# Optimization experiments

Hardware: AMD Instinct MI355X
Metric: run time of the kernel (lower is better)

## Reference

```python
import jax, jax.numpy as jnp
import numpy as np

N_SRC0, N_DST0, N_E0 = 286000, 11000, 275000
N_DST1, N_E1 = 1000, 10000
IN_FEATS, N_HIDDEN, N_CLASSES = 602, 256, 41


def setup_inputs() -> dict:
    key = jax.random.key(0)
    ks = jax.random.split(key, 12)
    inp = {
        "x": jax.random.normal(ks[0], (N_SRC0, IN_FEATS), dtype=jnp.float32),
        "Wself0": jax.random.normal(ks[1], (IN_FEATS, N_HIDDEN), dtype=jnp.float32) * 0.05,
        "Wneigh0": jax.random.normal(ks[2], (IN_FEATS, N_HIDDEN), dtype=jnp.float32) * 0.05,
        "b0": jnp.zeros((N_HIDDEN,), dtype=jnp.float32),
        "Wself1": jax.random.normal(ks[3], (N_HIDDEN, N_CLASSES), dtype=jnp.float32) * 0.05,
        "Wneigh1": jax.random.normal(ks[4], (N_HIDDEN, N_CLASSES), dtype=jnp.float32) * 0.05,
        "b1": jnp.zeros((N_CLASSES,), dtype=jnp.float32),
        "e0_src": jax.random.randint(ks[5], (N_E0,), 0, N_SRC0, dtype=jnp.int64 if jax.config.jax_enable_x64 else jnp.int32),
        "e0_dst": jax.random.randint(ks[6], (N_E0,), 0, N_DST0, dtype=jnp.int64 if jax.config.jax_enable_x64 else jnp.int32),
        "e1_src": jax.random.randint(ks[7], (N_E1,), 0, N_DST0, dtype=jnp.int64 if jax.config.jax_enable_x64 else jnp.int32),
        "e1_dst": jax.random.randint(ks[8], (N_E1,), 0, N_DST1, dtype=jnp.int64 if jax.config.jax_enable_x64 else jnp.int32),
    }
    return inp


def _mean_agg(h, src, dst, n_dst):
    # gather neighbor feats along edges, segment-mean into dst nodes
    s = jax.ops.segment_sum(h[src], dst, num_segments=n_dst)  # [n_dst, d]
    cnt = jax.ops.segment_sum(jnp.ones_like(dst, dtype=h.dtype), dst, num_segments=n_dst)
    return s / jnp.maximum(cnt, 1.0)[:, None]


def reference(x, Wself0, Wneigh0, b0, Wself1, Wneigh1, b1, e0_src, e0_dst, e1_src, e1_dst):
    # Layer 0: SAGEConv mean over block0 (src=286000, dst=11000) + relu
    # (dropout is identity in eval mode)
    h_dst = x[:N_DST0]
    h_agg = _mean_agg(x, e0_src, e0_dst, N_DST0)
    h = h_dst @ Wself0 + h_agg @ Wneigh0 + b0
    h = jax.nn.relu(h)
    # Layer 1: SAGEConv mean over block1 (src=11000, dst=1000)
    h_dst1 = h[:N_DST1]
    h_agg1 = _mean_agg(h, e1_src, e1_dst, N_DST1)
    out = h_dst1 @ Wself1 + h_agg1 @ Wneigh1 + b1
    return out
```

## Files before the change

### kernel.cpp

```cpp
#include <hip/hip_runtime.h>

#define N_SRC0   286000
#define N_DST0   11000
#define N_E0     275000
#define N_DST1   1000
#define N_E1     10000
#define IN_FEATS 602
#define N_HIDDEN 256
#define N_CLASSES 41

#define KP 608
#define MP 11008
#define LDT 40

typedef unsigned short u16;
typedef __attribute__((ext_vector_type(8))) short short8;
typedef __attribute__((ext_vector_type(4))) float f32x4;

__device__ inline void split_bf16(float v, u16& hi, u16& lo) {
    unsigned u = __float_as_uint(v);
    unsigned r = u + 0x7FFFu + ((u >> 16) & 1u);
    hi = (u16)(r >> 16);
    float vhi = __uint_as_float((unsigned)hi << 16);
    float vl = v - vhi;
    unsigned u2 = __float_as_uint(vl);
    unsigned r2 = u2 + 0x7FFFu + ((u2 >> 16) & 1u);
    lo = (u16)(r2 >> 16);
}


__global__ void count_kernel(const int* __restrict__ d0, int n0, int* __restrict__ c0,
                             const int* __restrict__ d1, int n1, int* __restrict__ c1) {
    int i = blockIdx.x * blockDim.x + threadIdx.x;
    if (i < n0) {
        atomicAdd(&c0[d0[i]], 1);
    } else {
        int j = i - n0;
        if (j < n1) atomicAdd(&c1[d1[j]], 1);
    }
}

__global__ void scan_kernel(const int* __restrict__ cnt0, int* __restrict__ off0, int n0_,
                            const int* __restrict__ cnt1, int* __restrict__ off1, int n1_) {
    const int* cnt; int* off; int n;
    if (blockIdx.x == 0) { cnt = cnt0; off = off0; n = n0_; }
    else                 { cnt = cnt1; off = off1; n = n1_; }
    __shared__ int sums[1024];
    int tid = threadIdx.x;
    int chunk = (n + 1023) >> 10;
    int start = tid * chunk;
    int end = min(start + chunk, n);
    int s = 0;
    for (int i = start; i < end; i++) s += cnt[i];
    sums[tid] = s;
    __syncthreads();
    for (int d = 1; d < 1024; d <<= 1) {
        int v = (tid >= d) ? sums[tid - d] : 0;
        __syncthreads();
        sums[tid] += v;
        __syncthreads();
    }
    int run = (tid > 0) ? sums[tid - 1] : 0;
    for (int i = start; i < end; i++) { off[i] = run; run += cnt[i]; }
    if (tid == 1023) off[n] = run;
}

__global__ void fill_kernel(const int* __restrict__ s0, const int* __restrict__ d0, int n0,
                            const int* __restrict__ off0, int* __restrict__ cur0, int* __restrict__ csr0,
                            const int* __restrict__ s1, const int* __restrict__ d1, int n1,
                            const int* __restrict__ off1, int* __restrict__ cur1, int* __restrict__ csr1) {
    int i = blockIdx.x * blockDim.x + threadIdx.x;
    if (i < n0) {
        int d = d0[i];
        int p = atomicAdd(&cur0[d], 1);
        csr0[off0[d] + p] = s0[i];
    } else {
        int j = i - n0;
        if (j < n1) {
            int d = d1[j];
            int p = atomicAdd(&cur1[d], 1);
            csr1[off1[d] + p] = s1[j];
        }
    }
}

__global__ void xconv_kernel(const float* __restrict__ x,
                             u16* __restrict__ xhi, u16* __restrict__ xlo) {
    int idx = blockIdx.x * blockDim.x + threadIdx.x;
    if (idx >= N_DST0 * KP) return;
    int row = idx / KP, k = idx - row * KP;
    float v = (k < IN_FEATS) ? x[(size_t)row * IN_FEATS + k] : 0.f;
    u16 hi, lo; split_bf16(v, hi, lo);
    xhi[idx] = hi; xlo[idx] = lo;
}

__global__ void wconv_kernel(const float* __restrict__ Wself, const float* __restrict__ Wneigh,
                             u16* __restrict__ wt) {
    int idx = blockIdx.x * blockDim.x + threadIdx.x;
    if (idx >= 2 * KP * 256) return;
    int part = idx / (KP * 256);
    int rem  = idx - part * (KP * 256);
    int k = rem / 256;
    int n = rem - k * 256;
    float v = (k < IN_FEATS) ? (part ? Wneigh[(size_t)k * 256 + n] : Wself[(size_t)k * 256 + n]) : 0.f;
    u16 hi, lo; split_bf16(v, hi, lo);
    u16* base = wt + (size_t)part * 2 * 256 * KP;
    base[(size_t)n * KP + k] = hi;
    base[(size_t)256 * KP + (size_t)n * KP + k] = lo;
}

__global__ void agg0_kernel(const float* __restrict__ x, const int* __restrict__ off,
                            const int* __restrict__ csr,
                            u16* __restrict__ ahi, u16* __restrict__ alo) {
    int d = blockIdx.x;
    int tid = threadIdx.x;
    int c0 = tid, c1 = tid + 256, c2 = tid + 512;
    bool has2 = (c2 < IN_FEATS);
    float a0 = 0.f, a1 = 0.f, a2 = 0.f;
    int beg = off[d], end = off[d + 1];
    int e = beg;
    for (; e + 3 < end; e += 4) {
        const float* r0 = x + (size_t)csr[e]     * IN_FEATS;
        const float* r1 = x + (size_t)csr[e + 1] * IN_FEATS;
        const float* r2 = x + (size_t)csr[e + 2] * IN_FEATS;
        const float* r3 = x + (size_t)csr[e + 3] * IN_FEATS;
        float t00 = r0[c0], t10 = r1[c0], t20 = r2[c0], t30 = r3[c0];
        float t01 = r0[c1], t11 = r1[c1], t21 = r2[c1], t31 = r3[c1];
        float t02 = has2 ? r0[c2] : 0.f, t12 = has2 ? r1[c2] : 0.f;
        float t22 = has2 ? r2[c2] : 0.f, t32 = has2 ? r3[c2] : 0.f;
        a0 += (t00 + t10) + (t20 + t30);
        a1 += (t01 + t11) + (t21 + t31);
        a2 += (t02 + t12) + (t22 + t32);
    }
    for (; e < end; e++) {
        const float* r0 = x + (size_t)csr[e] * IN_FEATS;
        a0 += r0[c0];
        a1 += r0[c1];
        if (has2) a2 += r0[c2];
    }
    float inv = 1.f / fmaxf((float)(end - beg), 1.f);
    size_t base = (size_t)d * KP;
    u16 hi, lo;
    split_bf16(a0 * inv, hi, lo); ahi[base + c0] = hi; alo[base + c0] = lo;
    split_bf16(a1 * inv, hi, lo); ahi[base + c1] = hi; alo[base + c1] = lo;
    if (c2 < KP) {
        float v = has2 ? a2 * inv : 0.f;
        split_bf16(v, hi, lo); ahi[base + c2] = hi; alo[base + c2] = lo;
    }
}

__global__ __launch_bounds__(256) void layer0_mfma(
        const u16* __restrict__ xhi, const u16* __restrict__ xlo,
        const u16* __restrict__ ghi, const u16* __restrict__ glo,
        const u16* __restrict__ wt, const float* __restrict__ b,
        float* __restrict__ h) {
    __shared__ u16 Ahi[64][LDT], Alo[64][LDT], Bhi[64][LDT], Blo[64][LDT];
    const int t    = threadIdx.x;
    const int lane = t & 63;
    const int w    = t >> 6;
    const int wm   = w >> 1, wn = w & 1;
    const int row0 = blockIdx.x * 64;
    const int col0 = blockIdx.y * 64;
    const int sr   = t >> 2;
    const int sc   = (t & 3) * 8;
    const int fr   = lane & 15;
    const int ko   = (lane >> 4) * 8;

    f32x4 acc[2][2] = {};

    for (int part = 0; part < 2; part++) {
        const u16* Aphi = part ? ghi : xhi;
        const u16* Aplo = part ? glo : xlo;
        const u16* Bphi = wt + (size_t)part * 2 * 256 * KP;
        const u16* Bplo = Bphi + (size_t)256 * KP;
        for (int k0 = 0; k0 < KP; k0 += 32) {
            short8 va = *reinterpret_cast<const short8*>(&Aphi[(size_t)(row0 + sr) * KP + k0 + sc]);
            short8 vb = *reinterpret_cast<const short8*>(&Aplo[(size_t)(row0 + sr) * KP + k0 + sc]);
            short8 vc = *reinterpret_cast<const short8*>(&Bphi[(size_t)(col0 + sr) * KP + k0 + sc]);
            short8 vd = *reinterpret_cast<const short8*>(&Bplo[(size_t)(col0 + sr) * KP + k0 + sc]);
            __syncthreads();
            *reinterpret_cast<short8*>(&Ahi[sr][sc]) = va;
            *reinterpret_cast<short8*>(&Alo[sr][sc]) = vb;
            *reinterpret_cast<short8*>(&Bhi[sr][sc]) = vc;
            *reinterpret_cast<short8*>(&Blo[sr][sc]) = vd;
            __syncthreads();
            short8 bh[2], bl[2];
#pragma unroll
            for (int n = 0; n < 2; n++) {
                bh[n] = *reinterpret_cast<const short8*>(&Bhi[wn * 32 + n * 16 + fr][ko]);
                bl[n] = *reinterpret_cast<const short8*>(&Blo[wn * 32 + n * 16 + fr][ko]);
            }
#pragma unroll
            for (int m = 0; m < 2; m++) {
                short8 ah = *reinterpret_cast<const short8*>(&Ahi[wm * 32 + m * 16 + fr][ko]);
                short8 al = *reinterpret_cast<const short8*>(&Alo[wm * 32 + m * 16 + fr][ko]);
#pragma unroll
                for (int n = 0; n < 2; n++) {
                    acc[m][n] = __builtin_amdgcn_mfma_f32_16x16x32_bf16(ah, bh[n], acc[m][n], 0, 0, 0);
                    acc[m][n] = __builtin_amdgcn_mfma_f32_16x16x32_bf16(ah, bl[n], acc[m][n], 0, 0, 0);
                    acc[m][n] = __builtin_amdgcn_mfma_f32_16x16x32_bf16(al, bh[n], acc[m][n], 0, 0, 0);
                }
            }
        }
    }
    const int fq = lane >> 4;
#pragma unroll
    for (int m = 0; m < 2; m++) {
#pragma unroll
        for (int n = 0; n < 2; n++) {
            int gcol = col0 + wn * 32 + n * 16 + fr;
            float bc = b[gcol];
#pragma unroll
            for (int r = 0; r < 4; r++) {
                int grow = row0 + wm * 32 + m * 16 + fq * 4 + r;
                if (grow < N_DST0)
                    h[(size_t)grow * N_HIDDEN + gcol] = fmaxf(acc[m][n][r] + bc, 0.f);
            }
        }
    }
}

__global__ void agg1_kernel(const float* __restrict__ h, const int* __restrict__ off,
                            const int* __restrict__ csr, float* __restrict__ agg) {
    int d = blockIdx.x;
    int tid = threadIdx.x;
    float a = 0.f;
    int beg = off[d], end = off[d + 1];
    for (int e = beg; e < end; e++)
        a += h[(size_t)csr[e] * N_HIDDEN + tid];
    agg[(size_t)d * N_HIDDEN + tid] = a / fmaxf((float)(end - beg), 1.f);
}

__global__ void layer1_kernel(const float* __restrict__ h, const float* __restrict__ agg1,
                              const float* __restrict__ Wself, const float* __restrict__ Wneigh,
                              const float* __restrict__ b, float* __restrict__ out) {
    int idx = blockIdx.x * blockDim.x + threadIdx.x;
    if (idx >= N_DST1 * N_CLASSES) return;
    int d = idx / N_CLASSES, c = idx % N_CLASSES;
    const float* hd = h + (size_t)d * N_HIDDEN;
    const float* ha = agg1 + (size_t)d * N_HIDDEN;
    float acc = b[c];
    for (int k = 0; k < N_HIDDEN; k++)
        acc += hd[k] * Wself[k * N_CLASSES + c] + ha[k] * Wneigh[k * N_CLASSES + c];
    out[idx] = acc;
}

extern "C" void kernel_launch(void* const* d_in, const int* in_sizes, int n_in,
                              void* d_out, int out_size, void* d_ws, size_t ws_size,
                              hipStream_t stream) {
    const float* x       = (const float*)d_in[0];
    const float* Wself0  = (const float*)d_in[1];
    const float* Wneigh0 = (const float*)d_in[2];
    const float* b0      = (const float*)d_in[3];
    const float* Wself1  = (const float*)d_in[4];
    const float* Wneigh1 = (const float*)d_in[5];
    const float* b1      = (const float*)d_in[6];
    const int* e0_src = (const int*)d_in[7];
    const int* e0_dst = (const int*)d_in[8];
    const int* e1_src = (const int*)d_in[9];
    const int* e1_dst = (const int*)d_in[10];

    char* ws = (char*)d_ws;
    size_t o = 0;
    auto alloc = [&](size_t bytes) -> void* {
        void* p = ws + o;
        o = (o + bytes + 255) & ~(size_t)255;
        return p;
    };
    int* cnt_block = (int*)alloc((size_t)(N_DST0 + N_DST0 + N_DST1 + N_DST1) * sizeof(int));
    int* cnt0 = cnt_block;
    int* cur0 = cnt_block + N_DST0;
    int* cnt1 = cnt_block + 2 * N_DST0;
    int* cur1 = cnt_block + 2 * N_DST0 + N_DST1;
    int* off0 = (int*)alloc((size_t)(N_DST0 + 1) * sizeof(int));
    int* off1 = (int*)alloc((size_t)(N_DST1 + 1) * sizeof(int));
    int* csr0 = (int*)alloc((size_t)N_E0 * sizeof(int));
    int* csr1 = (int*)alloc((size_t)N_E1 * sizeof(int));
    u16* xhi = (u16*)alloc((size_t)MP * KP * sizeof(u16));
    u16* xlo = (u16*)alloc((size_t)MP * KP * sizeof(u16));
    u16* ahi = (u16*)alloc((size_t)MP * KP * sizeof(u16));
    u16* alo = (u16*)alloc((size_t)MP * KP * sizeof(u16));
    u16* wt  = (u16*)alloc((size_t)2 * 2 * 256 * KP * sizeof(u16));
    float* h    = (float*)alloc((size_t)N_DST0 * N_HIDDEN * sizeof(float));
    float* agg1 = (float*)alloc((size_t)N_DST1 * N_HIDDEN * sizeof(float));

    hipMemsetAsync(cnt_block, 0, (size_t)(2 * N_DST0 + 2 * N_DST1) * sizeof(int), stream);

    int total_e = N_E0 + N_E1;
    count_kernel<<<(total_e + 255) / 256, 256, 0, stream>>>(e0_dst, N_E0, cnt0, e1_dst, N_E1, cnt1);
    scan_kernel<<<2, 1024, 0, stream>>>(cnt0, off0, N_DST0, cnt1, off1, N_DST1);
    fill_kernel<<<(total_e + 255) / 256, 256, 0, stream>>>(e0_src, e0_dst, N_E0, off0, cur0, csr0,
                                                           e1_src, e1_dst, N_E1, off1, cur1, csr1);
    xconv_kernel<<<(N_DST0 * KP + 255) / 256, 256, 0, stream>>>(x, xhi, xlo);
    wconv_kernel<<<(2 * KP * 256 + 255) / 256, 256, 0, stream>>>(Wself0, Wneigh0, wt);
    agg0_kernel<<<N_DST0, 256, 0, stream>>>(x, off0, csr0, ahi, alo);
    dim3 g0(MP / 64, N_HIDDEN / 64);
    layer0_mfma<<<g0, 256, 0, stream>>>(xhi, xlo, ahi, alo, wt, b0, h);
    agg1_kernel<<<N_DST1, 256, 0, stream>>>(h, off1, csr1, agg1);
    layer1_kernel<<<(N_DST1 * N_CLASSES + 255) / 256, 256, 0, stream>>>(h, agg1, Wself1, Wneigh1, b1,
                                                                        (float*)d_out);
}
```

Before: 1.001 ms.

## Fuse prep kernels, convert x inside GEMM, vectorize gather, fuse layer-1

Five separate changes. The edge-count pass and the weight conversion now share one launch. The separate x-to-bf16 conversion kernel is removed: layer0_mfma reads fp32 x directly and splits it into hi/lo while staging tiles, with a register prefetch of the next tile placed before the compute step. The layer-0 gather now uses float2 loads with two columns per thread and writes packed 32-bit stores. The layer-1 aggregation and output matmul are fused into one kernel through shared memory. Together these cut launches, intermediate buffers and global traffic, at the cost of redoing the conversion once per column-block in the GEMM and running a layer-1 matmul that uses only 41 of 256 threads.

```diff
diff --git a/kernel.cpp b/kernel.cpp
--- a/kernel.cpp
+++ b/kernel.cpp
@@ -28,15 +28,33 @@
     lo = (u16)(r2 >> 16);
 }
 
-
-__global__ void count_kernel(const int* __restrict__ d0, int n0, int* __restrict__ c0,
-                             const int* __restrict__ d1, int n1, int* __restrict__ c1) {
-    int i = blockIdx.x * blockDim.x + threadIdx.x;
-    if (i < n0) {
-        atomicAdd(&c0[d0[i]], 1);
+#define NB_COUNT ((N_E0 + N_E1 + 255) / 256)
+#define NB_WCONV ((2 * KP * 256) / 256)
+
+__global__ void prep_kernel(const int* __restrict__ d0, int* __restrict__ c0,
+                            const int* __restrict__ d1, int* __restrict__ c1,
+                            const float* __restrict__ Wself, const float* __restrict__ Wneigh,
+                            u16* __restrict__ wt) {
+    int bid = blockIdx.x;
+    if (bid < NB_COUNT) {
+        int i = bid * 256 + threadIdx.x;
+        if (i < N_E0) {
+            atomicAdd(&c0[d0[i]], 1);
+        } else {
+            int j = i - N_E0;
+            if (j < N_E1) atomicAdd(&c1[d1[j]], 1);
+        }
     } else {
-        int j = i - n0;
-        if (j < n1) atomicAdd(&c1[d1[j]], 1);
+        int idx = (bid - NB_COUNT) * 256 + threadIdx.x;
+        int part = idx / (KP * 256);
+        int rem  = idx - part * (KP * 256);
+        int k = rem / 256;
+        int n = rem - k * 256;
+        float v = (k < IN_FEATS) ? (part ? Wneigh[(size_t)k * 256 + n] : Wself[(size_t)k * 256 + n]) : 0.f;
+        u16 hi, lo; split_bf16(v, hi, lo);
+        u16* base = wt + (size_t)part * 2 * 256 * KP;
+        base[(size_t)n * KP + k] = hi;
+        base[(size_t)256 * KP + (size_t)n * KP + k] = lo;
     }
 }
 
@@ -84,73 +102,56 @@
     }
 }
 
-__global__ void xconv_kernel(const float* __restrict__ x,
-                             u16* __restrict__ xhi, u16* __restrict__ xlo) {
-    int idx = blockIdx.x * blockDim.x + threadIdx.x;
-    if (idx >= N_DST0 * KP) return;
-    int row = idx / KP, k = idx - row * KP;
-    float v = (k < IN_FEATS) ? x[(size_t)row * IN_FEATS + k] : 0.f;
-    u16 hi, lo; split_bf16(v, hi, lo);
-    xhi[idx] = hi; xlo[idx] = lo;
-}
-
-__global__ void wconv_kernel(const float* __restrict__ Wself, const float* __restrict__ Wneigh,
-                             u16* __restrict__ wt) {
-    int idx = blockIdx.x * blockDim.x + threadIdx.x;
-    if (idx >= 2 * KP * 256) return;
-    int part = idx / (KP * 256);
-    int rem  = idx - part * (KP * 256);
-    int k = rem / 256;
-    int n = rem - k * 256;
-    float v = (k < IN_FEATS) ? (part ? Wneigh[(size_t)k * 256 + n] : Wself[(size_t)k * 256 + n]) : 0.f;
-    u16 hi, lo; split_bf16(v, hi, lo);
-    u16* base = wt + (size_t)part * 2 * 256 * KP;
-    base[(size_t)n * KP + k] = hi;
-    base[(size_t)256 * KP + (size_t)n * KP + k] = lo;
-}
-
 __global__ void agg0_kernel(const float* __restrict__ x, const int* __restrict__ off,
                             const int* __restrict__ csr,
                             u16* __restrict__ ahi, u16* __restrict__ alo) {
     int d = blockIdx.x;
-    int tid = threadIdx.x;
-    int c0 = tid, c1 = tid + 256, c2 = tid + 512;
-    bool has2 = (c2 < IN_FEATS);
-    float a0 = 0.f, a1 = 0.f, a2 = 0.f;
+    int t = threadIdx.x;
+    const bool has1 = (t < 45);
+    const float2* X = (const float2*)x;
+    float a0x = 0.f, a0y = 0.f, a1x = 0.f, a1y = 0.f;
     int beg = off[d], end = off[d + 1];
     int e = beg;
     for (; e + 3 < end; e += 4) {
-        const float* r0 = x + (size_t)csr[e]     * IN_FEATS;
-        const float* r1 = x + (size_t)csr[e + 1] * IN_FEATS;
-        const float* r2 = x + (size_t)csr[e + 2] * IN_FEATS;
-        const float* r3 = x + (size_t)csr[e + 3] * IN_FEATS;
-        float t00 = r0[c0], t10 = r1[c0], t20 = r2[c0], t30 = r3[c0];
-        float t01 = r0[c1], t11 = r1[c1], t21 = r2[c1], t31 = r3[c1];
-        float t02 = has2 ? r0[c2] : 0.f, t12 = has2 ? r1[c2] : 0.f;
-        float t22 = has2 ? r2[c2] : 0.f, t32 = has2 ? r3[c2] : 0.f;
-        a0 += (t00 + t10) + (t20 + t30);
-        a1 += (t01 + t11) + (t21 + t31);
-        a2 += (t02 + t12) + (t22 + t32);
+        const float2* p0 = X + (size_t)csr[e]     * 301;
+        const float2* p1 = X + (size_t)csr[e + 1] * 301;
+        const float2* p2 = X + (size_t)csr[e + 2] * 301;
+        const float2* p3 = X + (size_t)csr[e + 3] * 301;
+        float2 u0 = p0[t], u1 = p1[t], u2 = p2[t], u3 = p3[t];
+        if (has1) {
+            float2 w0 = p0[256 + t], w1 = p1[256 + t], w2 = p2[256 + t], w3 = p3[256 + t];
+            a1x += (w0.x + w1.x) + (w2.x + w3.x);
+            a1y += (w0.y + w1.y) + (w2.y + w3.y);
+        }
+        a0x += (u0.x + u1.x) + (u2.x + u3.x);
+        a0y += (u0.y + u1.y) + (u2.y + u3.y);
     }
     for (; e < end; e++) {
-        const float* r0 = x + (size_t)csr[e] * IN_FEATS;
-        a0 += r0[c0];
-        a1 += r0[c1];
-        if (has2) a2 += r0[c2];
+        const float2* p0 = X + (size_t)csr[e] * 301;
+        float2 u0 = p0[t];
+        a0x += u0.x; a0y += u0.y;
+        if (has1) { float2 w0 = p0[256 + t]; a1x += w0.x; a1y += w0.y; }
     }
     float inv = 1.f / fmaxf((float)(end - beg), 1.f);
     size_t base = (size_t)d * KP;
-    u16 hi, lo;
-    split_bf16(a0 * inv, hi, lo); ahi[base + c0] = hi; alo[base + c0] = lo;
-    split_bf16(a1 * inv, hi, lo); ahi[base + c1] = hi; alo[base + c1] = lo;
-    if (c2 < KP) {
-        float v = has2 ? a2 * inv : 0.f;
-        split_bf16(v, hi, lo); ahi[base + c2] = hi; alo[base + c2] = lo;
+    u16 h0, l0, h1, l1;
+    split_bf16(a0x * inv, h0, l0);
+    split_bf16(a0y * inv, h1, l1);
+    *(unsigned*)&ahi[base + 2 * t] = (unsigned)h0 | ((unsigned)h1 << 16);
+    *(unsigned*)&alo[base + 2 * t] = (unsigned)l0 | ((unsigned)l1 << 16);
+    if (has1) {
+        split_bf16(a1x * inv, h0, l0);
+        split_bf16(a1y * inv, h1, l1);
+        *(unsigned*)&ahi[base + 512 + 2 * t] = (unsigned)h0 | ((unsigned)h1 << 16);
+        *(unsigned*)&alo[base + 512 + 2 * t] = (unsigned)l0 | ((unsigned)l1 << 16);
+    } else if (t < 48) {
+        *(unsigned*)&ahi[base + 512 + 2 * t] = 0u;
+        *(unsigned*)&alo[base + 512 + 2 * t] = 0u;
     }
 }
 
 __global__ __launch_bounds__(256) void layer0_mfma(
-        const u16* __restrict__ xhi, const u16* __restrict__ xlo,
+        const float* __restrict__ x,
         const u16* __restrict__ ghi, const u16* __restrict__ glo,
         const u16* __restrict__ wt, const float* __restrict__ b,
         float* __restrict__ h) {
@@ -166,43 +167,91 @@
     const int fr   = lane & 15;
     const int ko   = (lane >> 4) * 8;
 
+    const u16* wt0 = wt;
+    const u16* wt1 = wt + (size_t)2 * 256 * KP;
+
     f32x4 acc[2][2] = {};
 
-    for (int part = 0; part < 2; part++) {
-        const u16* Aphi = part ? ghi : xhi;
-        const u16* Aplo = part ? glo : xlo;
-        const u16* Bphi = wt + (size_t)part * 2 * 256 * KP;
-        const u16* Bplo = Bphi + (size_t)256 * KP;
-        for (int k0 = 0; k0 < KP; k0 += 32) {
-            short8 va = *reinterpret_cast<const short8*>(&Aphi[(size_t)(row0 + sr) * KP + k0 + sc]);
-            short8 vb = *reinterpret_cast<const short8*>(&Aplo[(size_t)(row0 + sr) * KP + k0 + sc]);
-            short8 vc = *reinterpret_cast<const short8*>(&Bphi[(size_t)(col0 + sr) * KP + k0 + sc]);
-            short8 vd = *reinterpret_cast<const short8*>(&Bplo[(size_t)(col0 + sr) * KP + k0 + sc]);
-            __syncthreads();
-            *reinterpret_cast<short8*>(&Ahi[sr][sc]) = va;
-            *reinterpret_cast<short8*>(&Alo[sr][sc]) = vb;
-            *reinterpret_cast<short8*>(&Bhi[sr][sc]) = vc;
-            *reinterpret_cast<short8*>(&Blo[sr][sc]) = vd;
-            __syncthreads();
-            short8 bh[2], bl[2];
+    float2 fa[4];
+    short8 pah, pal;
+    short8 pbh, pbl;
+
+    auto load0 = [&](int k0) {
+        const float* ap = x + (size_t)(row0 + sr) * IN_FEATS + k0 + sc;
+        fa[0] = *(const float2*)(ap + 0);
+        fa[1] = *(const float2*)(ap + 2);
+        fa[2] = *(const float2*)(ap + 4);
+        fa[3] = *(const float2*)(ap + 6);
+        const u16* bp = wt0 + (size_t)(col0 + sr) * KP + k0 + sc;
+        pbh = *(const short8*)bp;
+        pbl = *(const short8*)(bp + (size_t)256 * KP);
+    };
+    auto load1 = [&](int k0) {
+        size_t ao = (size_t)(row0 + sr) * KP + k0 + sc;
+        pah = *(const short8*)(ghi + ao);
+        pal = *(const short8*)(glo + ao);
+        const u16* bp = wt1 + (size_t)(col0 + sr) * KP + k0 + sc;
+        pbh = *(const short8*)bp;
+        pbl = *(const short8*)(bp + (size_t)256 * KP);
+    };
+    auto store0 = [&]() {
+        short8 hv, lv;
+#pragma unroll
+        for (int j = 0; j < 4; j++) {
+            u16 h0, l0, h1, l1;
+            split_bf16(fa[j].x, h0, l0);
+            split_bf16(fa[j].y, h1, l1);
+            hv[2 * j] = (short)h0; hv[2 * j + 1] = (short)h1;
+            lv[2 * j] = (short)l0; lv[2 * j + 1] = (short)l1;
+        }
+        *(short8*)&Ahi[sr][sc] = hv;
+        *(short8*)&Alo[sr][sc] = lv;
+        *(short8*)&Bhi[sr][sc] = pbh;
+        *(short8*)&Blo[sr][sc] = pbl;
+    };
+    auto store1 = [&]() {
+        *(short8*)&Ahi[sr][sc] = pah;
+        *(short8*)&Alo[sr][sc] = pal;
+        *(short8*)&Bhi[sr][sc] = pbh;
+        *(short8*)&Blo[sr][sc] = pbl;
+    };
+    auto compute = [&]() {
+        short8 bh[2], bl[2];
+#pragma unroll
+        for (int n = 0; n < 2; n++) {
+            bh[n] = *(const short8*)&Bhi[wn * 32 + n * 16 + fr][ko];
+            bl[n] = *(const short8*)&Blo[wn * 32 + n * 16 + fr][ko];
+        }
+#pragma unroll
+        for (int m = 0; m < 2; m++) {
+            short8 ah = *(const short8*)&Ahi[wm * 32 + m * 16 + fr][ko];
+            short8 al = *(const short8*)&Alo[wm * 32 + m * 16 + fr][ko];
 #pragma unroll
             for (int n = 0; n < 2; n++) {
-                bh[n] = *reinterpret_cast<const short8*>(&Bhi[wn * 32 + n * 16 + fr][ko]);
-                bl[n] = *reinterpret_cast<const short8*>(&Blo[wn * 32 + n * 16 + fr][ko]);
+                acc[m][n] = __builtin_amdgcn_mfma_f32_16x16x32_bf16(ah, bh[n], acc[m][n], 0, 0, 0);
+                acc[m][n] = __builtin_amdgcn_mfma_f32_16x16x32_bf16(ah, bl[n], acc[m][n], 0, 0, 0);
+                acc[m][n] = __builtin_amdgcn_mfma_f32_16x16x32_bf16(al, bh[n], acc[m][n], 0, 0, 0);
             }
-#pragma unroll
-            for (int m = 0; m < 2; m++) {
-                short8 ah = *reinterpret_cast<const short8*>(&Ahi[wm * 32 + m * 16 + fr][ko]);
-                short8 al = *reinterpret_cast<const short8*>(&Alo[wm * 32 + m * 16 + fr][ko]);
-#pragma unroll
-                for (int n = 0; n < 2; n++) {
-                    acc[m][n] = __builtin_amdgcn_mfma_f32_16x16x32_bf16(ah, bh[n], acc[m][n], 0, 0, 0);
-                    acc[m][n] = __builtin_amdgcn_mfma_f32_16x16x32_bf16(ah, bl[n], acc[m][n], 0, 0, 0);
-                    acc[m][n] = __builtin_amdgcn_mfma_f32_16x16x32_bf16(al, bh[n], acc[m][n], 0, 0, 0);
-                }
-            }
-        }
-    }
+        }
+    };
+
+    load0(0);
+    for (int s = 0; s < KP / 32; s++) {
+        __syncthreads();
+        store0();
+        __syncthreads();
+        if (s < KP / 32 - 1) load0((s + 1) * 32);
+        else                 load1(0);
+        compute();
+    }
+    for (int s = 0; s < KP / 32; s++) {
+        __syncthreads();
+        store1();
+        __syncthreads();
+        if (s < KP / 32 - 1) load1((s + 1) * 32);
+        compute();
+    }
+
     const int fq = lane >> 4;
 #pragma unroll
     for (int m = 0; m < 2; m++) {
@@ -220,29 +269,26 @@
     }
 }
 
-__global__ void agg1_kernel(const float* __restrict__ h, const int* __restrict__ off,
-                            const int* __restrict__ csr, float* __restrict__ agg) {
+__global__ __launch_bounds__(256) void fused_l1(
+        const float* __restrict__ h, const int* __restrict__ off, const int* __restrict__ csr,
+        const float* __restrict__ Wself, const float* __restrict__ Wneigh,
+        const float* __restrict__ b, float* __restrict__ out) {
+    __shared__ float sh[N_HIDDEN], sa[N_HIDDEN];
     int d = blockIdx.x;
-    int tid = threadIdx.x;
+    int t = threadIdx.x;
     float a = 0.f;
     int beg = off[d], end = off[d + 1];
     for (int e = beg; e < end; e++)
-        a += h[(size_t)csr[e] * N_HIDDEN + tid];
-    agg[(size_t)d * N_HIDDEN + tid] = a / fmaxf((float)(end - beg), 1.f);
-}
-
-__global__ void layer1_kernel(const float* __restrict__ h, const float* __restrict__ agg1,
-                              const float* __restrict__ Wself, const float* __restrict__ Wneigh,
-                              const float* __restrict__ b, float* __restrict__ out) {
-    int idx = blockIdx.x * blockDim.x + threadIdx.x;
-    if (idx >= N_DST1 * N_CLASSES) return;
-    int d = idx / N_CLASSES, c = idx % N_CLASSES;
-    const float* hd = h + (size_t)d * N_HIDDEN;
-    const float* ha = agg1 + (size_t)d * N_HIDDEN;
-    float acc = b[c];
-    for (int k = 0; k < N_HIDDEN; k++)
-        acc += hd[k] * Wself[k * N_CLASSES + c] + ha[k] * Wneigh[k * N_CLASSES + c];
-    out[idx] = acc;
+        a += h[(size_t)csr[e] * N_HIDDEN + t];
+    sa[t] = a / fmaxf((float)(end - beg), 1.f);
+    sh[t] = h[(size_t)d * N_HIDDEN + t];
+    __syncthreads();
+    if (t < N_CLASSES) {
+        float acc = b[t];
+        for (int k = 0; k < N_HIDDEN; k++)
+            acc += sh[k] * Wself[k * N_CLASSES + t] + sa[k] * Wneigh[k * N_CLASSES + t];
+        out[(size_t)d * N_CLASSES + t] = acc;
+    }
 }
 
 extern "C" void kernel_launch(void* const* d_in, const int* in_sizes, int n_in,
@@ -276,27 +322,21 @@
     int* off1 = (int*)alloc((size_t)(N_DST1 + 1) * sizeof(int));
     int* csr0 = (int*)alloc((size_t)N_E0 * sizeof(int));
     int* csr1 = (int*)alloc((size_t)N_E1 * sizeof(int));
-    u16* xhi = (u16*)alloc((size_t)MP * KP * sizeof(u16));
-    u16* xlo = (u16*)alloc((size_t)MP * KP * sizeof(u16));
     u16* ahi = (u16*)alloc((size_t)MP * KP * sizeof(u16));
     u16* alo = (u16*)alloc((size_t)MP * KP * sizeof(u16));
     u16* wt  = (u16*)alloc((size_t)2 * 2 * 256 * KP * sizeof(u16));
-    float* h    = (float*)alloc((size_t)N_DST0 * N_HIDDEN * sizeof(float));
-    float* agg1 = (float*)alloc((size_t)N_DST1 * N_HIDDEN * sizeof(float));
+    float* h = (float*)alloc((size_t)N_DST0 * N_HIDDEN * sizeof(float));
 
     hipMemsetAsync(cnt_block, 0, (size_t)(2 * N_DST0 + 2 * N_DST1) * sizeof(int), stream);
 
     int total_e = N_E0 + N_E1;
-    count_kernel<<<(total_e + 255) / 256, 256, 0, stream>>>(e0_dst, N_E0, cnt0, e1_dst, N_E1, cnt1);
+    prep_kernel<<<NB_COUNT + NB_WCONV, 256, 0, stream>>>(e0_dst, cnt0, e1_dst, cnt1,
+                                                         Wself0, Wneigh0, wt);
     scan_kernel<<<2, 1024, 0, stream>>>(cnt0, off0, N_DST0, cnt1, off1, N_DST1);
     fill_kernel<<<(total_e + 255) / 256, 256, 0, stream>>>(e0_src, e0_dst, N_E0, off0, cur0, csr0,
                                                            e1_src, e1_dst, N_E1, off1, cur1, csr1);
-    xconv_kernel<<<(N_DST0 * KP + 255) / 256, 256, 0, stream>>>(x, xhi, xlo);
-    wconv_kernel<<<(2 * KP * 256 + 255) / 256, 256, 0, stream>>>(Wself0, Wneigh0, wt);
     agg0_kernel<<<N_DST0, 256, 0, stream>>>(x, off0, csr0, ahi, alo);
     dim3 g0(MP / 64, N_HIDDEN / 64);
-    layer0_mfma<<<g0, 256, 0, stream>>>(xhi, xlo, ahi, alo, wt, b0, h);
-    agg1_kernel<<<N_DST1, 256, 0, stream>>>(h, off1, csr1, agg1);
-    layer1_kernel<<<(N_DST1 * N_CLASSES + 255) / 256, 256, 0, stream>>>(h, agg1, Wself1, Wneigh1, b1,
-                                                                        (float*)d_out);
-}
+    layer0_mfma<<<g0, 256, 0, stream>>>(x, ahi, alo, wt, b0, h);
+    fused_l1<<<N_DST1, 256, 0, stream>>>(h, off1, csr1, Wself1, Wneigh1, b1, (float*)d_out);
+}
```

After: 978.1 us. -2.2%, faster.
